# Performance work log

Hardware: AMD Instinct MI355X
Metric: run time of the kernel (lower is better)

The kernel has to match this reference:

```python
import jax, jax.numpy as jnp
import numpy as np

NUM_HEADS = 8

def _qkv(t, W, b, H):
    # t: [B, L, C] -> q, k, v each [B, H, L, D]
    B, L, C = t.shape
    D = C // H
    qkv = (t @ W + b).reshape(B, L, 3, H, D)
    qkv = jnp.moveaxis(qkv, 2, 0)           # [3, B, L, H, D]
    qkv = jnp.swapaxes(qkv, 2, 3)           # [3, B, H, L, D]
    return qkv[0], qkv[1], qkv[2]

def _attend(q, k, v, scale):
    # q,k,v: [B, H, L, D] -> [B, L, C]
    B, H, L, D = q.shape
    scores = jnp.einsum('bhqd,bhkd->bhqk', q, k) * scale
    attn = jax.nn.softmax(scores, axis=-1)
    out = jnp.einsum('bhqk,bhkd->bhqd', attn, v)
    return jnp.swapaxes(out, 1, 2).reshape(B, L, H * D)

def setup_inputs() -> dict:
    key = jax.random.key(0)
    ks = jax.random.split(key, 7)
    B, N, C = 8, 2048, 512
    s_in = 1.0 / np.sqrt(C)
    return {
        'x': jax.random.normal(ks[0], (B, N, C), dtype=jnp.float32),
        'W_rgb_qkv': jax.random.normal(ks[1], (C, 3 * C), dtype=jnp.float32) * s_in,
        'b_rgb_qkv': jax.random.normal(ks[2], (3 * C,), dtype=jnp.float32) * 0.02,
        'W_depth_qkv': jax.random.normal(ks[3], (C, 3 * C), dtype=jnp.float32) * s_in,
        'b_depth_qkv': jax.random.normal(ks[4], (3 * C,), dtype=jnp.float32) * 0.02,
        'W_proj': jax.random.normal(ks[5], (C, C), dtype=jnp.float32) * s_in,
        'b_proj': jax.random.normal(ks[6], (C,), dtype=jnp.float32) * 0.02,
    }

def reference(x, W_rgb_qkv, b_rgb_qkv, W_depth_qkv, b_depth_qkv, W_proj, b_proj):
    B, N, C = x.shape
    H = NUM_HEADS
    D = C // H
    scale = D ** -0.5
    L = N // 2
    rgb, depth = x[:, :L], x[:, L:]
    rq, rk, rv = _qkv(rgb, W_rgb_qkv, b_rgb_qkv, H)
    dq, dk, dv = _qkv(depth, W_depth_qkv, b_depth_qkv, H)
    # rgb queries attend to depth K/V (named depth_v in torch code)
    depth_out = _attend(rq, dk, dv, scale)
    # depth queries attend to rgb K/V (named rgb_v in torch code)
    rgb_out = _attend(dq, rk, rv, scale)
    out = jnp.concatenate([rgb_out, depth_out], axis=1)  # [B, N, C]
    return out @ W_proj + b_proj
```

## Files before the change

kernel.cpp:

```cpp
#include <hip/hip_runtime.h>
#include <hip/hip_bf16.h>

typedef __attribute__((ext_vector_type(8))) short s16x8;
typedef __attribute__((ext_vector_type(4))) float f32x4;

__device__ __forceinline__ ushort f2bf(float f) {
  union { float f; unsigned int u; } c; c.f = f;
  unsigned int u = c.u + 0x7fffu + ((c.u >> 16) & 1u);
  return (ushort)(u >> 16);
}

__device__ __forceinline__ unsigned int pack2(float lo, float hi) {
  __hip_bfloat162 b2 = __float22bfloat162_rn(make_float2(lo, hi));
  union { __hip_bfloat162 b; unsigned int u; } c; c.b = b2;
  return c.u;
}

__device__ __forceinline__ s16x8 ld16(const ushort* p) {
  union { uint4 u; s16x8 s; } c;
  c.u = *reinterpret_cast<const uint4*>(p);
  return c.s;
}

__device__ __forceinline__ f32x4 mfma16(s16x8 a, s16x8 b, f32x4 c) {
  return __builtin_amdgcn_mfma_f32_16x16x32_bf16(a, b, c, 0, 0, 0);
}

__device__ __forceinline__ float exp2fast(float x) { return __builtin_amdgcn_exp2f(x); }

__device__ __forceinline__ void gld_lds16(const void* g, void* l) {
  __builtin_amdgcn_global_load_lds(
      (const __attribute__((address_space(1))) void*)g,
      (__attribute__((address_space(3))) void*)l, 16, 0, 0);
}


__global__ __launch_bounds__(256) void k_prep(
    const float* __restrict__ x, ushort* __restrict__ xb,
    const float* __restrict__ Wr, ushort* __restrict__ WtR,
    const float* __restrict__ Wd, ushort* __restrict__ WtD,
    const float* __restrict__ Wp, ushort* __restrict__ WtP) {
  __shared__ float tile[32][33];
  int b = blockIdx.x, t = threadIdx.x;
  if (b < 8192) {
    int i = (b * 256 + t) * 4;
    float4 v = *reinterpret_cast<const float4*>(x + i);
    ushort4 o;
    o.x = f2bf(v.x); o.y = f2bf(v.y); o.z = f2bf(v.z); o.w = f2bf(v.w);
    *reinterpret_cast<ushort4*>(xb + i) = o;
    return;
  }
  b -= 8192;
  const float* src; ushort* dst; int N;
  if (b < 768)      { src = Wr; dst = WtR; N = 1536; }
  else if (b < 1536){ b -= 768;  src = Wd; dst = WtD; N = 1536; }
  else              { b -= 1536; src = Wp; dst = WtP; N = 512; }
  int nb = N >> 5;
  int n0 = (b % nb) * 32, k0 = (b / nb) * 32;
  int tx = t & 31, ty = t >> 5;
#pragma unroll
  for (int i = 0; i < 32; i += 8)
    tile[ty + i][tx] = src[(k0 + ty + i) * N + (n0 + tx)];
  __syncthreads();
#pragma unroll
  for (int i = 0; i < 32; i += 8)
    dst[(size_t)(n0 + ty + i) * 512 + (k0 + tx)] = f2bf(tile[tx][ty + i]);
}


__device__ __forceinline__ void stage_lds(const ushort* __restrict__ src, int ld,
                                          char* ldsbase, int t) {
#pragma unroll
  for (int p = 0; p < 4; ++p) {
    int chunk = p * 256 + t;
    int r = chunk >> 3, cc = chunk & 7;
    gld_lds16(src + r * ld + ((cc ^ (r & 7)) * 8), ldsbase + (chunk & ~63) * 16);
  }
}

__device__ __forceinline__ s16x8 lds_frag(const char* lds, int row, int c) {
  union { uint4 u; s16x8 s; } cv;
  cv.u = *reinterpret_cast<const uint4*>(lds + row * 128 + ((c ^ (row & 7)) * 16));
  return cv.s;
}


template <bool TRANS>
__global__ __launch_bounds__(256) void k_qkv(
    const ushort* __restrict__ xb, const ushort* __restrict__ WtR,
    const ushort* __restrict__ WtD, const float* __restrict__ bR,
    const float* __restrict__ bD, ushort* __restrict__ Qb,
    ushort* __restrict__ Kb, ushort* __restrict__ Vt) {
  __shared__ __align__(16) char lds[65536];
  int m0 = blockIdx.x * 128;
  int n0 = (TRANS ? 1024 : 0) + blockIdx.y * 128;
  int s = m0 >> 13, bb = (m0 >> 10) & 7, lbase = m0 & 1023;
  const ushort* A = xb + (size_t)(bb * 2048 + s * 1024 + lbase) * 512;
  const ushort* Wt = (s ? WtD : WtR) + (size_t)n0 * 512;
  const float* bias = s ? bD : bR;
  int t = threadIdx.x;
  int wid = t >> 6, ln = t & 15, g = (t & 63) >> 4;
  int wr = wid >> 1, wc = wid & 1;
  f32x4 acc[4][4] = {};
  stage_lds(A, 512, lds, t);
  stage_lds(Wt, 512, lds + 16384, t);
  __syncthreads();
  for (int ks = 0; ks < 8; ++ks) {
    char* cbuf = lds + (ks & 1) * 32768;
    if (ks < 7) {
      char* nbuf = lds + ((ks + 1) & 1) * 32768;
      stage_lds(A + (ks + 1) * 64, 512, nbuf, t);
      stage_lds(Wt + (ks + 1) * 64, 512, nbuf + 16384, t);
    }
    char* ldsA = cbuf;
    char* ldsB = cbuf + 16384;
#pragma unroll
    for (int kk = 0; kk < 2; ++kk) {
      s16x8 af[4], bf[4];
#pragma unroll
      for (int mi = 0; mi < 4; ++mi) af[mi] = lds_frag(ldsA, wr * 64 + mi * 16 + ln, kk * 4 + g);
#pragma unroll
      for (int ni = 0; ni < 4; ++ni) bf[ni] = lds_frag(ldsB, wc * 64 + ni * 16 + ln, kk * 4 + g);
#pragma unroll
      for (int mi = 0; mi < 4; ++mi)
#pragma unroll
        for (int ni = 0; ni < 4; ++ni)
          acc[mi][ni] = TRANS ? mfma16(bf[ni], af[mi], acc[mi][ni])
                              : mfma16(af[mi], bf[ni], acc[mi][ni]);
    }
    __syncthreads();
  }
  int hb_base = (s * 8 + bb) * 8;
  if (!TRANS) {
    bool isK = (n0 >> 9) != 0;
    ushort* dst = isK ? Kb : Qb;
    float sc = isK ? 1.0f : 0.18033688011112042f;
#pragma unroll
    for (int mi = 0; mi < 4; ++mi)
#pragma unroll
      for (int ni = 0; ni < 4; ++ni) {
        f32x4 v = acc[mi][ni];
        int col = n0 + wc * 64 + ni * 16 + ln;
        int h = (col >> 6) & 7, d = col & 63;
        float bv = bias[col];
        ushort* hp = dst + ((size_t)(hb_base + h) << 16);
        int lr = lbase + wr * 64 + mi * 16 + g * 4;
#pragma unroll
        for (int j = 0; j < 4; ++j) hp[(lr + j) * 64 + d] = f2bf((v[j] + bv) * sc);
      }
  } else {
    ushort* et = (ushort*)lds;
#pragma unroll
    for (int mi = 0; mi < 4; ++mi) {
      int ll = wr * 64 + mi * 16 + ln;
      int lpl = (ll & ~63) | (ll & 0x23) | ((ll & 0x0C) << 1) | ((ll & 0x10) >> 2);
      int chunk = lpl >> 3, within = lpl & 7;
#pragma unroll
      for (int ni = 0; ni < 4; ++ni) {
        f32x4 v = acc[mi][ni];
        int crb = wc * 64 + ni * 16 + g * 4;
#pragma unroll
        for (int j = 0; j < 4; ++j) {
          int cr = crb + j;
          float bv = bias[n0 + cr];
          *(ushort*)((char*)et + cr * 256 + ((chunk ^ (cr & 15)) * 16) + within * 2)
              = f2bf(v[j] + bv);
        }
      }
    }
    __syncthreads();
#pragma unroll
    for (int pass = 0; pass < 8; ++pass) {
      int rrow = pass * 16 + (t >> 4);
      int c16 = t & 15;
      int col = n0 + rrow;
      int h = (col >> 6) & 7, d = col & 63;
      uint4 vv = *(const uint4*)((const char*)et + rrow * 256 + ((c16 ^ (rrow & 15)) * 16));
      *reinterpret_cast<uint4*>(Vt + ((size_t)(hb_base + h) << 16) + d * 1024 + lbase + c16 * 8)
          = vv;
    }
  }
}


__global__ __launch_bounds__(512) void k_attn(const ushort* __restrict__ Qb,
                                              const ushort* __restrict__ Kb,
                                              const ushort* __restrict__ Vt,
                                              ushort* __restrict__ AO) {
  __shared__ __align__(16) char lds[49152];
  int bid = blockIdx.x;
  int set = bid & 127, qb = bid >> 7;
  int pair = set & 1, h = (set >> 1) & 7, bb = set >> 4;
  int sQ = 1 - pair, sKV = pair;
  const ushort* Qp = Qb + ((size_t)((sQ * 8 + bb) * 8 + h) << 16);
  const ushort* Kp = Kb + ((size_t)((sKV * 8 + bb) * 8 + h) << 16);
  const ushort* Vp = Vt + ((size_t)((sKV * 8 + bb) * 8 + h) << 16);
  int t = threadIdx.x, w = t >> 6, ln = t & 15, g = (t & 63) >> 4;
  int q0 = qb * 256 + w * 32;
  s16x8 qf0a = ld16(Qp + (q0 + ln) * 64 + g * 8);
  s16x8 qf1a = ld16(Qp + (q0 + ln) * 64 + 32 + g * 8);
  s16x8 qf0b = ld16(Qp + (q0 + 16 + ln) * 64 + g * 8);
  s16x8 qf1b = ld16(Qp + (q0 + 16 + ln) * 64 + 32 + g * 8);

  int r = t >> 3, cc = t & 7;
  int kof = r * 64 + ((cc ^ (r & 7)) * 8);
  int vof = r * 1024 + ((cc ^ (r & 7)) * 8);
  int ldst = (t & ~63) * 16;

  float ls_a = 0.f, ls_b = 0.f;
  f32x4 oca[4] = {}, ocb[4] = {};

  const ushort* kstage = Kp;
  const ushort* vstage = Vp;

  char* bc = lds;
  char* bn = lds + 16384;
  char* bs = lds + 32768;

  gld_lds16(kstage + kof, bc + ldst);
  gld_lds16(vstage + vof, bc + 8192 + ldst);
  kstage += 4096; vstage += 64;
  gld_lds16(kstage + kof, bn + ldst);
  gld_lds16(vstage + vof, bn + 8192 + ldst);
  kstage += 4096; vstage += 64;
  asm volatile("s_waitcnt vmcnt(2)" ::: "memory");
  __builtin_amdgcn_sched_barrier(0);
  __builtin_amdgcn_s_barrier();
  __builtin_amdgcn_sched_barrier(0);

  for (int it = 0; it < 16; ++it) {
    if (it < 14) {
      gld_lds16(kstage + kof, bs + ldst);
      gld_lds16(vstage + vof, bs + 8192 + ldst);
      kstage += 4096; vstage += 64;
    }

    f32x4 za[4], zb[4];
    __builtin_amdgcn_s_setprio(1);
#pragma unroll
    for (int s = 0; s < 4; ++s) {
      s16x8 k0 = lds_frag(bc, s * 16 + ln, g);
      s16x8 k1 = lds_frag(bc, s * 16 + ln, 4 + g);
      f32x4 z1 = {}; z1 = mfma16(k0, qf0a, z1); z1 = mfma16(k1, qf1a, z1); za[s] = z1;
      f32x4 z2 = {}; z2 = mfma16(k0, qf0b, z2); z2 = mfma16(k1, qf1b, z2); zb[s] = z2;
    }
    __builtin_amdgcn_s_setprio(0);

    unsigned int pwa[8], pwb[8];
#pragma unroll
    for (int s = 0; s < 4; ++s) {
      float p0 = exp2fast(za[s][0]), p1 = exp2fast(za[s][1]);
      float p2 = exp2fast(za[s][2]), p3 = exp2fast(za[s][3]);
      ls_a += (p0 + p1) + (p2 + p3);
      pwa[2 * s] = pack2(p0, p1); pwa[2 * s + 1] = pack2(p2, p3);
      float r0 = exp2fast(zb[s][0]), r1 = exp2fast(zb[s][1]);
      float r2 = exp2fast(zb[s][2]), r3 = exp2fast(zb[s][3]);
      ls_b += (r0 + r1) + (r2 + r3);
      pwb[2 * s] = pack2(r0, r1); pwb[2 * s + 1] = pack2(r2, r3);
    }
    union { uint4 u; s16x8 v; } c0, c1, c2, c3;
    c0.u = make_uint4(pwa[0], pwa[1], pwa[2], pwa[3]);
    c1.u = make_uint4(pwa[4], pwa[5], pwa[6], pwa[7]);
    c2.u = make_uint4(pwb[0], pwb[1], pwb[2], pwb[3]);
    c3.u = make_uint4(pwb[4], pwb[5], pwb[6], pwb[7]);
    s16x8 pf0a = c0.v, pf1a = c1.v, pf0b = c2.v, pf1b = c3.v;

    __builtin_amdgcn_s_setprio(1);
#pragma unroll
    for (int d = 0; d < 4; ++d) {
      s16x8 v0 = lds_frag(bc + 8192, d * 16 + ln, g);
      s16x8 v1 = lds_frag(bc + 8192, d * 16 + ln, 4 + g);
      oca[d] = mfma16(v0, pf0a, oca[d]);
      oca[d] = mfma16(v1, pf1a, oca[d]);
      ocb[d] = mfma16(v0, pf0b, ocb[d]);
      ocb[d] = mfma16(v1, pf1b, ocb[d]);
    }
    __builtin_amdgcn_s_setprio(0);

    if (it < 15) {
      if (it < 14) {
        asm volatile("s_waitcnt vmcnt(2)" ::: "memory");
      } else {
        asm volatile("s_waitcnt vmcnt(0)" ::: "memory");
      }
      __builtin_amdgcn_sched_barrier(0);
      __builtin_amdgcn_s_barrier();
      __builtin_amdgcn_sched_barrier(0);
    }
    char* tmp = bc; bc = bn; bn = bs; bs = tmp;
  }

  ls_a += __shfl_xor(ls_a, 16, 64);
  ls_a += __shfl_xor(ls_a, 32, 64);
  ls_b += __shfl_xor(ls_b, 16, 64);
  ls_b += __shfl_xor(ls_b, 32, 64);
  float inva = 1.0f / ls_a, invb = 1.0f / ls_b;
  int orow = bb * 2048 + pair * 1024 + q0 + ln;
#pragma unroll
  for (int d = 0; d < 4; ++d) {
    uint2 st;
    st.x = pack2(oca[d][0] * inva, oca[d][1] * inva);
    st.y = pack2(oca[d][2] * inva, oca[d][3] * inva);
    *reinterpret_cast<uint2*>(AO + (size_t)orow * 512 + h * 64 + d * 16 + 4 * g) = st;
    uint2 st2;
    st2.x = pack2(ocb[d][0] * invb, ocb[d][1] * invb);
    st2.y = pack2(ocb[d][2] * invb, ocb[d][3] * invb);
    *reinterpret_cast<uint2*>(AO + (size_t)(orow + 16) * 512 + h * 64 + d * 16 + 4 * g) = st2;
  }
}


__global__ __launch_bounds__(256) void k_gemm_proj(const ushort* __restrict__ AO,
                                                   const ushort* __restrict__ WtP,
                                                   const float* __restrict__ bP,
                                                   float* __restrict__ Out) {
  __shared__ __align__(16) char lds[65536];
  int m0 = blockIdx.x * 128, n0 = blockIdx.y * 128;
  const ushort* A = AO + (size_t)m0 * 512;
  const ushort* Wt = WtP + (size_t)n0 * 512;
  int t = threadIdx.x;
  int wid = t >> 6, ln = t & 15, g = (t & 63) >> 4;
  int wr = wid >> 1, wc = wid & 1;
  f32x4 acc[4][4] = {};
  stage_lds(A, 512, lds, t);
  stage_lds(Wt, 512, lds + 16384, t);
  __syncthreads();
  for (int ks = 0; ks < 8; ++ks) {
    char* cbuf = lds + (ks & 1) * 32768;
    if (ks < 7) {
      char* nbuf = lds + ((ks + 1) & 1) * 32768;
      stage_lds(A + (ks + 1) * 64, 512, nbuf, t);
      stage_lds(Wt + (ks + 1) * 64, 512, nbuf + 16384, t);
    }
    char* ldsA = cbuf;
    char* ldsB = cbuf + 16384;
#pragma unroll
    for (int kk = 0; kk < 2; ++kk) {
      s16x8 af[4], bf[4];
#pragma unroll
      for (int mi = 0; mi < 4; ++mi) af[mi] = lds_frag(ldsA, wr * 64 + mi * 16 + ln, kk * 4 + g);
#pragma unroll
      for (int ni = 0; ni < 4; ++ni) bf[ni] = lds_frag(ldsB, wc * 64 + ni * 16 + ln, kk * 4 + g);
#pragma unroll
      for (int mi = 0; mi < 4; ++mi)
#pragma unroll
        for (int ni = 0; ni < 4; ++ni) acc[mi][ni] = mfma16(af[mi], bf[ni], acc[mi][ni]);
    }
    __syncthreads();
  }
#pragma unroll
  for (int mi = 0; mi < 4; ++mi)
#pragma unroll
    for (int ni = 0; ni < 4; ++ni) {
      f32x4 v = acc[mi][ni];
      int col = n0 + wc * 64 + ni * 16 + ln;
      float bv = bP[col];
      int r0 = m0 + wr * 64 + mi * 16 + g * 4;
#pragma unroll
      for (int j = 0; j < 4; ++j) Out[(size_t)(r0 + j) * 512 + col] = v[j] + bv;
    }
}


extern "C" void kernel_launch(void* const* d_in, const int* in_sizes, int n_in,
                              void* d_out, int out_size, void* d_ws, size_t ws_size,
                              hipStream_t stream) {
  const float* x      = (const float*)d_in[0];
  const float* W_rgb  = (const float*)d_in[1];
  const float* b_rgb  = (const float*)d_in[2];
  const float* W_dep  = (const float*)d_in[3];
  const float* b_dep  = (const float*)d_in[4];
  const float* W_proj = (const float*)d_in[5];
  const float* b_proj = (const float*)d_in[6];
  float* out = (float*)d_out;

  char* ws = (char*)d_ws;
  ushort* xb  = (ushort*)(ws + 0);
  ushort* WtR = (ushort*)(ws + 16777216);
  ushort* WtD = (ushort*)(ws + 18350080);
  ushort* WtP = (ushort*)(ws + 19922944);
  ushort* Qb  = (ushort*)(ws + 20447232);
  ushort* Kb  = (ushort*)(ws + 37224448);
  ushort* Vt  = (ushort*)(ws + 54001664);
  ushort* AO  = (ushort*)(ws + 70778880);

  k_prep<<<9984, 256, 0, stream>>>(x, xb, W_rgb, WtR, W_dep, WtD, W_proj, WtP);
  k_qkv<false><<<dim3(128, 8), 256, 0, stream>>>(xb, WtR, WtD, b_rgb, b_dep, Qb, Kb, Vt);
  k_qkv<true><<<dim3(128, 4), 256, 0, stream>>>(xb, WtR, WtD, b_rgb, b_dep, Qb, Kb, Vt);
  k_attn<<<512, 512, 0, stream>>>(Qb, Kb, Vt, AO);
  k_gemm_proj<<<dim3(128, 4), 256, 0, stream>>>(AO, WtP, b_proj, out);
}
```

Baseline: 137.8 us.

## Triple-buffer QKV GEMM with BK=32 and halve per-wave query rows in attention

```diff
diff --git a/kernel.cpp b/kernel.cpp
--- a/kernel.cpp
+++ b/kernel.cpp
@@ -68,6 +68,18 @@
 }
 
 
+__device__ __forceinline__ s16x8 lds_frag(const char* lds, int row, int c) {
+  union { uint4 u; s16x8 s; } cv;
+  cv.u = *reinterpret_cast<const uint4*>(lds + row * 128 + ((c ^ (row & 7)) * 16));
+  return cv.s;
+}
+
+__device__ __forceinline__ s16x8 lds_frag32(const char* lds, int row, int c) {
+  union { uint4 u; s16x8 s; } cv;
+  cv.u = *reinterpret_cast<const uint4*>(lds + row * 64 + ((c ^ ((row >> 1) & 3)) * 16));
+  return cv.s;
+}
+
 __device__ __forceinline__ void stage_lds(const ushort* __restrict__ src, int ld,
                                           char* ldsbase, int t) {
 #pragma unroll
@@ -76,12 +88,6 @@
     int r = chunk >> 3, cc = chunk & 7;
     gld_lds16(src + r * ld + ((cc ^ (r & 7)) * 8), ldsbase + (chunk & ~63) * 16);
   }
-}
-
-__device__ __forceinline__ s16x8 lds_frag(const char* lds, int row, int c) {
-  union { uint4 u; s16x8 s; } cv;
-  cv.u = *reinterpret_cast<const uint4*>(lds + row * 128 + ((c ^ (row & 7)) * 16));
-  return cv.s;
 }
 
 
@@ -91,7 +97,7 @@
     const ushort* __restrict__ WtD, const float* __restrict__ bR,
     const float* __restrict__ bD, ushort* __restrict__ Qb,
     ushort* __restrict__ Kb, ushort* __restrict__ Vt) {
-  __shared__ __align__(16) char lds[65536];
+  __shared__ __align__(16) char lds[49152];
   int m0 = blockIdx.x * 128;
   int n0 = (TRANS ? 1024 : 0) + blockIdx.y * 128;
   int s = m0 >> 13, bb = (m0 >> 10) & 7, lbase = m0 & 1023;
@@ -101,35 +107,71 @@
   int t = threadIdx.x;
   int wid = t >> 6, ln = t & 15, g = (t & 63) >> 4;
   int wr = wid >> 1, wc = wid & 1;
+
+  int r0 = t >> 2, c0 = t & 3;
+  int r1 = (t + 256) >> 2, c1 = t & 3;
+  int so0 = r0 * 512 + ((c0 ^ ((r0 >> 1) & 3)) * 8);
+  int so1 = r1 * 512 + ((c1 ^ ((r1 >> 1) & 3)) * 8);
+  int ldu = (t & ~63) * 16;
+
+  const ushort* As = A;
+  const ushort* Bs = Wt;
+  char* b0 = lds;
+  char* b1 = lds + 16384;
+  char* b2 = lds + 32768;
+
   f32x4 acc[4][4] = {};
-  stage_lds(A, 512, lds, t);
-  stage_lds(Wt, 512, lds + 16384, t);
-  __syncthreads();
-  for (int ks = 0; ks < 8; ++ks) {
-    char* cbuf = lds + (ks & 1) * 32768;
-    if (ks < 7) {
-      char* nbuf = lds + ((ks + 1) & 1) * 32768;
-      stage_lds(A + (ks + 1) * 64, 512, nbuf, t);
-      stage_lds(Wt + (ks + 1) * 64, 512, nbuf + 16384, t);
-    }
-    char* ldsA = cbuf;
-    char* ldsB = cbuf + 16384;
-#pragma unroll
-    for (int kk = 0; kk < 2; ++kk) {
-      s16x8 af[4], bf[4];
-#pragma unroll
-      for (int mi = 0; mi < 4; ++mi) af[mi] = lds_frag(ldsA, wr * 64 + mi * 16 + ln, kk * 4 + g);
-#pragma unroll
-      for (int ni = 0; ni < 4; ++ni) bf[ni] = lds_frag(ldsB, wc * 64 + ni * 16 + ln, kk * 4 + g);
-#pragma unroll
-      for (int mi = 0; mi < 4; ++mi)
-#pragma unroll
-        for (int ni = 0; ni < 4; ++ni)
-          acc[mi][ni] = TRANS ? mfma16(bf[ni], af[mi], acc[mi][ni])
-                              : mfma16(af[mi], bf[ni], acc[mi][ni]);
-    }
-    __syncthreads();
-  }
+
+  gld_lds16(As + so0, b0 + ldu);
+  gld_lds16(As + so1, b0 + 4096 + ldu);
+  gld_lds16(Bs + so0, b0 + 8192 + ldu);
+  gld_lds16(Bs + so1, b0 + 12288 + ldu);
+  As += 32; Bs += 32;
+  gld_lds16(As + so0, b1 + ldu);
+  gld_lds16(As + so1, b1 + 4096 + ldu);
+  gld_lds16(Bs + so0, b1 + 8192 + ldu);
+  gld_lds16(Bs + so1, b1 + 12288 + ldu);
+  As += 32; Bs += 32;
+  asm volatile("s_waitcnt vmcnt(4)" ::: "memory");
+  __builtin_amdgcn_sched_barrier(0);
+  __builtin_amdgcn_s_barrier();
+  __builtin_amdgcn_sched_barrier(0);
+
+  for (int ks = 0; ks < 16; ++ks) {
+    if (ks < 14) {
+      gld_lds16(As + so0, b2 + ldu);
+      gld_lds16(As + so1, b2 + 4096 + ldu);
+      gld_lds16(Bs + so0, b2 + 8192 + ldu);
+      gld_lds16(Bs + so1, b2 + 12288 + ldu);
+      As += 32; Bs += 32;
+    }
+    s16x8 af[4], bf[4];
+    __builtin_amdgcn_s_setprio(1);
+#pragma unroll
+    for (int mi = 0; mi < 4; ++mi) af[mi] = lds_frag32(b0, wr * 64 + mi * 16 + ln, g);
+#pragma unroll
+    for (int ni = 0; ni < 4; ++ni) bf[ni] = lds_frag32(b0 + 8192, wc * 64 + ni * 16 + ln, g);
+#pragma unroll
+    for (int mi = 0; mi < 4; ++mi)
+#pragma unroll
+      for (int ni = 0; ni < 4; ++ni)
+        acc[mi][ni] = TRANS ? mfma16(bf[ni], af[mi], acc[mi][ni])
+                            : mfma16(af[mi], bf[ni], acc[mi][ni]);
+    __builtin_amdgcn_s_setprio(0);
+
+    if (ks < 15) {
+      if (ks < 14) {
+        asm volatile("s_waitcnt vmcnt(4)" ::: "memory");
+      } else {
+        asm volatile("s_waitcnt vmcnt(0)" ::: "memory");
+      }
+      __builtin_amdgcn_sched_barrier(0);
+      __builtin_amdgcn_s_barrier();
+      __builtin_amdgcn_sched_barrier(0);
+    }
+    char* tmp = b0; b0 = b1; b1 = b2; b2 = tmp;
+  }
+
   int hb_base = (s * 8 + bb) * 8;
   if (!TRANS) {
     bool isK = (n0 >> 9) != 0;
@@ -149,6 +191,7 @@
         for (int j = 0; j < 4; ++j) hp[(lr + j) * 64 + d] = f2bf((v[j] + bv) * sc);
       }
   } else {
+    __syncthreads();
     ushort* et = (ushort*)lds;
 #pragma unroll
     for (int mi = 0; mi < 4; ++mi) {
@@ -187,7 +230,7 @@
                                               const ushort* __restrict__ Kb,
                                               const ushort* __restrict__ Vt,
                                               ushort* __restrict__ AO) {
-  __shared__ __align__(16) char lds[49152];
+  __shared__ __align__(16) char lds[32768];
   int bid = blockIdx.x;
   int set = bid & 127, qb = bid >> 7;
   int pair = set & 1, h = (set >> 1) & 7, bb = set >> 4;
@@ -196,116 +239,91 @@
   const ushort* Kp = Kb + ((size_t)((sKV * 8 + bb) * 8 + h) << 16);
   const ushort* Vp = Vt + ((size_t)((sKV * 8 + bb) * 8 + h) << 16);
   int t = threadIdx.x, w = t >> 6, ln = t & 15, g = (t & 63) >> 4;
-  int q0 = qb * 256 + w * 32;
-  s16x8 qf0a = ld16(Qp + (q0 + ln) * 64 + g * 8);
-  s16x8 qf1a = ld16(Qp + (q0 + ln) * 64 + 32 + g * 8);
-  s16x8 qf0b = ld16(Qp + (q0 + 16 + ln) * 64 + g * 8);
-  s16x8 qf1b = ld16(Qp + (q0 + 16 + ln) * 64 + 32 + g * 8);
+  int q0 = qb * 128 + w * 16;
+  s16x8 qf0 = ld16(Qp + (q0 + ln) * 64 + g * 8);
+  s16x8 qf1 = ld16(Qp + (q0 + ln) * 64 + 32 + g * 8);
 
   int r = t >> 3, cc = t & 7;
   int kof = r * 64 + ((cc ^ (r & 7)) * 8);
   int vof = r * 1024 + ((cc ^ (r & 7)) * 8);
   int ldst = (t & ~63) * 16;
 
-  float ls_a = 0.f, ls_b = 0.f;
-  f32x4 oca[4] = {}, ocb[4] = {};
+  float ls = 0.f;
+  f32x4 oc[4] = {};
 
   const ushort* kstage = Kp;
   const ushort* vstage = Vp;
 
   char* bc = lds;
   char* bn = lds + 16384;
-  char* bs = lds + 32768;
 
   gld_lds16(kstage + kof, bc + ldst);
   gld_lds16(vstage + vof, bc + 8192 + ldst);
   kstage += 4096; vstage += 64;
-  gld_lds16(kstage + kof, bn + ldst);
-  gld_lds16(vstage + vof, bn + 8192 + ldst);
-  kstage += 4096; vstage += 64;
-  asm volatile("s_waitcnt vmcnt(2)" ::: "memory");
+  asm volatile("s_waitcnt vmcnt(0)" ::: "memory");
   __builtin_amdgcn_sched_barrier(0);
   __builtin_amdgcn_s_barrier();
   __builtin_amdgcn_sched_barrier(0);
 
   for (int it = 0; it < 16; ++it) {
-    if (it < 14) {
-      gld_lds16(kstage + kof, bs + ldst);
-      gld_lds16(vstage + vof, bs + 8192 + ldst);
+    if (it < 15) {
+      gld_lds16(kstage + kof, bn + ldst);
+      gld_lds16(vstage + vof, bn + 8192 + ldst);
       kstage += 4096; vstage += 64;
     }
 
-    f32x4 za[4], zb[4];
+    f32x4 z[4];
     __builtin_amdgcn_s_setprio(1);
 #pragma unroll
     for (int s = 0; s < 4; ++s) {
       s16x8 k0 = lds_frag(bc, s * 16 + ln, g);
       s16x8 k1 = lds_frag(bc, s * 16 + ln, 4 + g);
-      f32x4 z1 = {}; z1 = mfma16(k0, qf0a, z1); z1 = mfma16(k1, qf1a, z1); za[s] = z1;
-      f32x4 z2 = {}; z2 = mfma16(k0, qf0b, z2); z2 = mfma16(k1, qf1b, z2); zb[s] = z2;
+      f32x4 z1 = {}; z1 = mfma16(k0, qf0, z1); z1 = mfma16(k1, qf1, z1); z[s] = z1;
     }
     __builtin_amdgcn_s_setprio(0);
 
-    unsigned int pwa[8], pwb[8];
+    unsigned int pw[8];
 #pragma unroll
     for (int s = 0; s < 4; ++s) {
-      float p0 = exp2fast(za[s][0]), p1 = exp2fast(za[s][1]);
-      float p2 = exp2fast(za[s][2]), p3 = exp2fast(za[s][3]);
-      ls_a += (p0 + p1) + (p2 + p3);
-      pwa[2 * s] = pack2(p0, p1); pwa[2 * s + 1] = pack2(p2, p3);
-      float r0 = exp2fast(zb[s][0]), r1 = exp2fast(zb[s][1]);
-      float r2 = exp2fast(zb[s][2]), r3 = exp2fast(zb[s][3]);
-      ls_b += (r0 + r1) + (r2 + r3);
-      pwb[2 * s] = pack2(r0, r1); pwb[2 * s + 1] = pack2(r2, r3);
-    }
-    union { uint4 u; s16x8 v; } c0, c1, c2, c3;
-    c0.u = make_uint4(pwa[0], pwa[1], pwa[2], pwa[3]);
-    c1.u = make_uint4(pwa[4], pwa[5], pwa[6], pwa[7]);
-    c2.u = make_uint4(pwb[0], pwb[1], pwb[2], pwb[3]);
-    c3.u = make_uint4(pwb[4], pwb[5], pwb[6], pwb[7]);
-    s16x8 pf0a = c0.v, pf1a = c1.v, pf0b = c2.v, pf1b = c3.v;
+      float p0 = exp2fast(z[s][0]), p1 = exp2fast(z[s][1]);
+      float p2 = exp2fast(z[s][2]), p3 = exp2fast(z[s][3]);
+      ls += (p0 + p1) + (p2 + p3);
+      pw[2 * s] = pack2(p0, p1); pw[2 * s + 1] = pack2(p2, p3);
+    }
+    union { uint4 u; s16x8 v; } c0, c1;
+    c0.u = make_uint4(pw[0], pw[1], pw[2], pw[3]);
+    c1.u = make_uint4(pw[4], pw[5], pw[6], pw[7]);
+    s16x8 pf0 = c0.v, pf1 = c1.v;
 
     __builtin_amdgcn_s_setprio(1);
 #pragma unroll
     for (int d = 0; d < 4; ++d) {
       s16x8 v0 = lds_frag(bc + 8192, d * 16 + ln, g);
       s16x8 v1 = lds_frag(bc + 8192, d * 16 + ln, 4 + g);
-      oca[d] = mfma16(v0, pf0a, oca[d]);
-      oca[d] = mfma16(v1, pf1a, oca[d]);
-      ocb[d] = mfma16(v0, pf0b, ocb[d]);
-      ocb[d] = mfma16(v1, pf1b, ocb[d]);
+      oc[d] = mfma16(v0, pf0, oc[d]);
+      oc[d] = mfma16(v1, pf1, oc[d]);
     }
     __builtin_amdgcn_s_setprio(0);
 
     if (it < 15) {
-      if (it < 14) {
-        asm volatile("s_waitcnt vmcnt(2)" ::: "memory");
-      } else {
-        asm volatile("s_waitcnt vmcnt(0)" ::: "memory");
-      }
+      asm volatile("s_waitcnt vmcnt(0)" ::: "memory");
       __builtin_amdgcn_sched_barrier(0);
       __builtin_amdgcn_s_barrier();
       __builtin_amdgcn_sched_barrier(0);
     }
-    char* tmp = bc; bc = bn; bn = bs; bs = tmp;
-  }
-
-  ls_a += __shfl_xor(ls_a, 16, 64);
-  ls_a += __shfl_xor(ls_a, 32, 64);
-  ls_b += __shfl_xor(ls_b, 16, 64);
-  ls_b += __shfl_xor(ls_b, 32, 64);
-  float inva = 1.0f / ls_a, invb = 1.0f / ls_b;
+    char* tmp = bc; bc = bn; bn = tmp;
+  }
+
+  ls += __shfl_xor(ls, 16, 64);
+  ls += __shfl_xor(ls, 32, 64);
+  float inv = 1.0f / ls;
   int orow = bb * 2048 + pair * 1024 + q0 + ln;
 #pragma unroll
   for (int d = 0; d < 4; ++d) {
     uint2 st;
-    st.x = pack2(oca[d][0] * inva, oca[d][1] * inva);
-    st.y = pack2(oca[d][2] * inva, oca[d][3] * inva);
+    st.x = pack2(oc[d][0] * inv, oc[d][1] * inv);
+    st.y = pack2(oc[d][2] * inv, oc[d][3] * inv);
     *reinterpret_cast<uint2*>(AO + (size_t)orow * 512 + h * 64 + d * 16 + 4 * g) = st;
-    uint2 st2;
-    st2.x = pack2(ocb[d][0] * invb, ocb[d][1] * invb);
-    st2.y = pack2(ocb[d][2] * invb, ocb[d][3] * invb);
-    *reinterpret_cast<uint2*>(AO + (size_t)(orow + 16) * 512 + h * 64 + d * 16 + 4 * g) = st2;
   }
 }
 
@@ -387,6 +405,6 @@
   k_prep<<<9984, 256, 0, stream>>>(x, xb, W_rgb, WtR, W_dep, WtD, W_proj, WtP);
   k_qkv<false><<<dim3(128, 8), 256, 0, stream>>>(xb, WtR, WtD, b_rgb, b_dep, Qb, Kb, Vt);
   k_qkv<true><<<dim3(128, 4), 256, 0, stream>>>(xb, WtR, WtD, b_rgb, b_dep, Qb, Kb, Vt);
-  k_attn<<<512, 512, 0, stream>>>(Qb, Kb, Vt, AO);
+  k_attn<<<1024, 512, 0, stream>>>(Qb, Kb, Vt, AO);
   k_gemm_proj<<<dim3(128, 4), 256, 0, stream>>>(AO, WtP, b_proj, out);
 }
```

After: 131.6 us, median of 2. 1.05x faster.
